# Kernel tuning notes

Hardware: AMD Instinct MI355X
Metric: run time of the kernel (lower is better)

Reference implementation:

```python
import jax, jax.numpy as jnp
import numpy as np

D_MODEL = 1024
N_HEADS = 16
HEAD_DIM = D_MODEL // N_HEADS
ROPE_THETA = 10000.0


def setup_inputs() -> dict:
    key = jax.random.key(0)
    ks = jax.random.split(key, 5)
    B, S = 4, 2048
    x = jax.random.normal(ks[0], (B, S, D_MODEL), dtype=jnp.float32)
    Wq = jax.random.normal(ks[1], (D_MODEL, D_MODEL), dtype=jnp.float32) * 0.02
    Wk = jax.random.normal(ks[2], (D_MODEL, D_MODEL), dtype=jnp.float32) * 0.02
    Wv = jax.random.normal(ks[3], (D_MODEL, D_MODEL), dtype=jnp.float32) * 0.02
    Wo = jax.random.normal(ks[4], (D_MODEL, D_MODEL), dtype=jnp.float32) * 0.02
    token_positions = jnp.arange(S, dtype=jnp.int32)
    return {"x": x, "token_positions": token_positions, "Wq": Wq, "Wk": Wk, "Wv": Wv, "Wo": Wo}


def apply_rope(t, positions):
    # t: [B, H, S, Dk]; positions: [S]
    half = HEAD_DIM // 2
    inv_freq = 1.0 / (ROPE_THETA ** (jnp.arange(half, dtype=jnp.float32) * 2.0 / HEAD_DIM))
    angles = positions.astype(jnp.float32)[:, None] * inv_freq[None, :]  # [S, half]
    cos = jnp.cos(angles)[None, None]  # [1,1,S,half]
    sin = jnp.sin(angles)[None, None]
    t_even = t[..., 0::2]
    t_odd = t[..., 1::2]
    rot_even = t_even * cos - t_odd * sin
    rot_odd = t_even * sin + t_odd * cos
    out = jnp.stack([rot_even, rot_odd], axis=-1)  # [B,H,S,half,2]
    return out.reshape(t.shape)


def reference(x, token_positions, Wq, Wk, Wv, Wo):
    B, S, _ = x.shape
    H, Dk = N_HEADS, HEAD_DIM
    # QKV projections, split heads -> [B, H, S, Dk]
    q = (x @ Wq).reshape(B, S, H, Dk).transpose(0, 2, 1, 3)
    k = (x @ Wk).reshape(B, S, H, Dk).transpose(0, 2, 1, 3)
    v = (x @ Wv).reshape(B, S, H, Dk).transpose(0, 2, 1, 3)
    q = apply_rope(q, token_positions)
    k = apply_rope(k, token_positions)
    scale = 1.0 / jnp.sqrt(jnp.asarray(Dk, dtype=x.dtype))
    scores = jnp.einsum('bhqd,bhkd->bhqk', q, k) * scale
    causal = jnp.tril(jnp.ones((S, S), dtype=bool))
    scores = jnp.where(causal[None, None], scores, jnp.asarray(-jnp.inf, dtype=scores.dtype))
    attn = jax.nn.softmax(scores, axis=-1)
    ctx = jnp.einsum('bhqk,bhkd->bhqd', attn, v)  # [B,H,S,Dk]
    ctx = ctx.transpose(0, 2, 1, 3).reshape(B, S, H * Dk)
    return ctx @ Wo
```

## Files before the change

kernel.cpp:

```cpp
#include <hip/hip_runtime.h>

typedef unsigned short u16;
typedef unsigned int   u32;
typedef __bf16  bf16x8 __attribute__((ext_vector_type(8)));
typedef float   f32x4  __attribute__((ext_vector_type(4)));
typedef float   f32x16 __attribute__((ext_vector_type(16)));
typedef u16     u16x4  __attribute__((ext_vector_type(4)));
typedef u16     u16x8  __attribute__((ext_vector_type(8)));
typedef u32     u32x4  __attribute__((ext_vector_type(4)));

#define D_MODEL 1024
#define N_HEADS 16
#define HEAD_DIM 64
#define BATCH 4
#define SEQ 2048
#define MROWS (BATCH*SEQ)

__device__ __forceinline__ u16 f2bf(float f){
  unsigned u = __builtin_bit_cast(unsigned, f);
  u += 0x7fffu + ((u >> 16) & 1u);
  return (u16)(u >> 16);
}
__device__ __forceinline__ float bf2f(u16 h){
  unsigned u = ((unsigned)h) << 16;
  return __builtin_bit_cast(float, u);
}
__device__ __forceinline__ u32 cvtpk(float a, float b){
  u32 r; asm("v_cvt_pk_bf16_f32 %0, %1, %2" : "=v"(r) : "v"(a), "v"(b)); return r;
}
__device__ __forceinline__ void gload_lds16(const u16* g, u16* l){
  __builtin_amdgcn_global_load_lds((const __attribute__((address_space(1))) void*)g,
                                   (__attribute__((address_space(3))) void*)l, 16, 0, 0);
}
#define MFMA16(a,b,c) __builtin_amdgcn_mfma_f32_16x16x32_bf16((a),(b),(c),0,0,0)

__global__ void k_cvt_x(const float* __restrict__ x, u16* __restrict__ xb, int n4){
  int i = blockIdx.x * 256 + threadIdx.x;
  if (i >= n4) return;
  float4 v = reinterpret_cast<const float4*>(x)[i];
  u16x4 o;
  o.x = f2bf(v.x); o.y = f2bf(v.y); o.z = f2bf(v.z); o.w = f2bf(v.w);
  *reinterpret_cast<u16x4*>(xb + (size_t)i * 4) = o;
}

__global__ void k_transpose_w(const float* __restrict__ Wq, const float* __restrict__ Wk,
                              const float* __restrict__ Wv, const float* __restrict__ Wo,
                              u16* __restrict__ wt){
  __shared__ float t[32][33];
  int z = blockIdx.z;
  const float* W = (z==0)?Wq:(z==1)?Wk:(z==2)?Wv:Wo;
  u16* O = wt + (size_t)z * (D_MODEL*(size_t)D_MODEL);
  int n0 = blockIdx.x*32, k0 = blockIdx.y*32;
  int tx = threadIdx.x, ty = threadIdx.y;
  #pragma unroll
  for (int i = ty; i < 32; i += 8) t[i][tx] = W[(size_t)(k0+i)*D_MODEL + n0 + tx];
  __syncthreads();
  #pragma unroll
  for (int i = ty; i < 32; i += 8){
    int n = n0 + i;
    int np = n;
    if (z < 2){ int d = n & 63; np = (n & ~63) | ((d & 1) << 5) | (d >> 1); }
    O[(size_t)np*D_MODEL + k0 + tx] = f2bf(t[tx][i]);
  }
}

__global__ void k_rope_tab(const int* __restrict__ pos, float2* __restrict__ tab){
  int i = blockIdx.x * 256 + threadIdx.x;
  int s = i >> 5, f = i & 31;
  float inv = exp2f(-(float)f * (13.287712379549449f / 32.0f));
  float a = (float)pos[s] * inv;
  float sn, cs;
  sincosf(a, &sn, &cs);
  tab[i] = make_float2(cs, sn);
}

__global__ __launch_bounds__(512, 4) void k_gqkv(const u16* __restrict__ A, const u16* __restrict__ Bt,
                                                 const float2* __restrict__ tab,
                                                 u16* __restrict__ qout, u16* __restrict__ kout,
                                                 u16* __restrict__ vout){
  __shared__ u16 sh[3*12288];
  const int tid = threadIdx.x, lane = tid & 63, w = tid >> 6;
  const int lr = lane & 15, lg = lane >> 4;
  const int m0 = blockIdx.x * 128, n0 = blockIdx.y * 256;
  const int wm = w >> 2, wn = w & 3;
  const int ra = tid >> 2;
  const int sca = ((tid & 3) ^ ((ra >> 1) & 3)) << 3;
  const u16* gA  = A  + (size_t)(m0 + ra)*1024 + sca;
  const u16* gB0 = Bt + (size_t)(n0 + ra)*1024 + sca;
  const int rb1 = 128 + ra;
  const u16* gB1 = Bt + (size_t)(n0 + rb1)*1024 + (((tid & 3) ^ ((rb1 >> 1) & 3)) << 3);
  const int dA  = w*512;
  const int dB0 = 4096 + w*512;
  const int dB1 = 8192 + w*512;
  int aoff[4], boff[4];
  #pragma unroll
  for (int mi = 0; mi < 4; ++mi){ int r_ = wm*64 + mi*16 + lr; aoff[mi] = r_*32 + ((lg ^ ((r_>>1)&3)) << 3); }
  #pragma unroll
  for (int ni = 0; ni < 4; ++ni){ int r_ = wn*64 + ni*16 + lr; boff[ni] = 4096 + r_*32 + ((lg ^ ((r_>>1)&3)) << 3); }

  f32x4 acc[4][4] = {};
#define SA_(base, t)  gload_lds16(gA  + (size_t)(t)*32, sh + (base) + dA)
#define SB0_(base, t) gload_lds16(gB0 + (size_t)(t)*32, sh + (base) + dB0)
#define SB1_(base, t) gload_lds16(gB1 + (size_t)(t)*32, sh + (base) + dB1)
  SA_(0,0); SB0_(0,0); SB1_(0,0);
  SA_(12288,1); SB0_(12288,1); SB1_(12288,1);
  int b0 = 0, b1 = 12288, b2 = 24576;
  #pragma unroll 1
  for (int t = 0; t < 32; ++t){
    if (t < 31) { asm volatile("s_waitcnt vmcnt(3) lgkmcnt(0)" ::: "memory"); }
    else        { asm volatile("s_waitcnt vmcnt(0) lgkmcnt(0)" ::: "memory"); }
    __builtin_amdgcn_s_barrier();
    __builtin_amdgcn_sched_barrier(0);
    const u16* Sb = sh + b0;
    bf16x8 af0 = *(const bf16x8*)&Sb[aoff[0]];
    bf16x8 af1 = *(const bf16x8*)&Sb[aoff[1]];
    bf16x8 af2 = *(const bf16x8*)&Sb[aoff[2]];
    bf16x8 af3 = *(const bf16x8*)&Sb[aoff[3]];
    bf16x8 vb0 = *(const bf16x8*)&Sb[boff[0]];
    bf16x8 vb1 = *(const bf16x8*)&Sb[boff[1]];
    if (t < 30){ SA_(b2, t+2); }
    __builtin_amdgcn_s_setprio(1);
    acc[0][0] = MFMA16(af0, vb0, acc[0][0]);
    acc[1][0] = MFMA16(af1, vb0, acc[1][0]);
    acc[2][0] = MFMA16(af2, vb0, acc[2][0]);
    acc[3][0] = MFMA16(af3, vb0, acc[3][0]);
    acc[0][1] = MFMA16(af0, vb1, acc[0][1]);
    acc[1][1] = MFMA16(af1, vb1, acc[1][1]);
    acc[2][1] = MFMA16(af2, vb1, acc[2][1]);
    acc[3][1] = MFMA16(af3, vb1, acc[3][1]);
    __builtin_amdgcn_s_setprio(0);
    bf16x8 vb2 = *(const bf16x8*)&Sb[boff[2]];
    bf16x8 vb3 = *(const bf16x8*)&Sb[boff[3]];
    if (t < 30){ SB0_(b2, t+2); SB1_(b2, t+2); }
    __builtin_amdgcn_s_setprio(1);
    acc[0][2] = MFMA16(af0, vb2, acc[0][2]);
    acc[1][2] = MFMA16(af1, vb2, acc[1][2]);
    acc[2][2] = MFMA16(af2, vb2, acc[2][2]);
    acc[3][2] = MFMA16(af3, vb2, acc[3][2]);
    acc[0][3] = MFMA16(af0, vb3, acc[0][3]);
    acc[1][3] = MFMA16(af1, vb3, acc[1][3]);
    acc[2][3] = MFMA16(af2, vb3, acc[2][3]);
    acc[3][3] = MFMA16(af3, vb3, acc[3][3]);
    __builtin_amdgcn_s_setprio(0);
    int tmp = b0; b0 = b1; b1 = b2; b2 = tmp;
  }
#undef SA_
#undef SB0_
#undef SB1_

  const int which = n0 >> 10;
  #pragma unroll
  for (int mi = 0; mi < 4; mi++){
    int row = m0 + wm*64 + mi*16 + lg*4;
    #pragma unroll
    for (int ni = 0; ni < 4; ni++){
      int col = n0 + wn*64 + ni*16 + lr;
      int cm = col & 1023;
      int hh = cm >> 6, d = cm & 63;
      f32x4 vv = acc[mi][ni];
      f32x4 vp = acc[mi][ni ^ 2];
      #pragma unroll
      for (int r = 0; r < 4; r++){
        int rr = row + r;
        int bb = rr >> 11, s = rr & (SEQ-1);
        float val = vv[r];
        if (which < 2){
          float e = (ni < 2) ? val : vp[r];
          float o = (ni < 2) ? vp[r] : val;
          float2 cs = tab[s*32 + ((ni & 1) << 4) + lr];
          float ov = (ni < 2) ? (e*cs.x - o*cs.y) : (e*cs.y + o*cs.x);
          if (which == 0){
            ov *= 0.18033688011112042f;
            qout[(size_t)rr*1024 + cm] = f2bf(ov);
          } else {
            kout[(((size_t)(bb*N_HEADS + hh))*SEQ + s)*64 + d] = f2bf(ov);
          }
        } else {
          vout[(((size_t)(bb*N_HEADS + hh))*(SEQ/16) + (s >> 4))*1024 + d*16 + (s & 15)] = f2bf(val);
        }
      }
    }
  }
}

__global__ __launch_bounds__(256, 4) void k_gemm3(const u16* __restrict__ A, const u16* __restrict__ Bt,
                                                  float* __restrict__ fout){
  __shared__ u16 sh[3*8192];
  const int K = 1024;
  int tid = threadIdx.x, lane = tid & 63, w = tid >> 6;
  int lr = lane & 15, lg = lane >> 4;
  int m0 = blockIdx.x * 128, n0 = blockIdx.y * 128;
  int wm = w >> 1, wn = w & 1;
  int srow = lane >> 2, scol = (lane & 3) * 8;
  const u16* ga = A  + (size_t)(m0 + w*16 + srow)*K + scol;
  const u16* gb = Bt + (size_t)(n0 + w*16 + srow)*K + scol;
  f32x4 acc[4][4] = {};

#define STG(off, t) { u16* Sb = sh + (off); \
    gload_lds16(ga + (size_t)(t)*32,        Sb + w*512); \
    gload_lds16(ga + (size_t)(t)*32 + 64*K, Sb + 2048 + w*512); \
    gload_lds16(gb + (size_t)(t)*32,        Sb + 4096 + w*512); \
    gload_lds16(gb + (size_t)(t)*32 + 64*K, Sb + 6144 + w*512); }

#define CMP(off) { const u16* Sb = sh + (off); \
    bf16x8 af[4], bv[4]; \
    _Pragma("unroll") \
    for (int mi = 0; mi < 4; mi++) \
      af[mi] = *(const bf16x8*)&Sb[(wm*64 + mi*16 + lr)*32 + lg*8]; \
    _Pragma("unroll") \
    for (int ni = 0; ni < 4; ni++) \
      bv[ni] = *(const bf16x8*)&Sb[4096 + (wn*64 + ni*16 + lr)*32 + lg*8]; \
    _Pragma("unroll") \
    for (int mi = 0; mi < 4; mi++){ \
      _Pragma("unroll") \
      for (int ni = 0; ni < 4; ni++) \
        acc[mi][ni] = MFMA16(af[mi], bv[ni], acc[mi][ni]); \
    } }

  STG(0, 0)
  STG(8192, 1)
  int oc = 0, on = 8192, os = 16384;
  #pragma unroll 1
  for (int t = 0; t < 31; ++t){
    asm volatile("s_waitcnt vmcnt(4) lgkmcnt(0)" ::: "memory");
    __builtin_amdgcn_s_barrier();
    __builtin_amdgcn_sched_barrier(0);
    if (t < 30){ STG(os, t+2) }
    CMP(oc)
    int tmp = oc; oc = on; on = os; os = tmp;
  }
  asm volatile("s_waitcnt vmcnt(0) lgkmcnt(0)" ::: "memory");
  __builtin_amdgcn_s_barrier();
  __builtin_amdgcn_sched_barrier(0);
  CMP(oc)
#undef STG
#undef CMP

  #pragma unroll
  for (int mi = 0; mi < 4; mi++){
    int row = m0 + wm*64 + mi*16 + lg*4;
    #pragma unroll
    for (int ni = 0; ni < 4; ni++){
      int col = n0 + wn*64 + ni*16 + lr;
      f32x4 vv = acc[mi][ni];
      #pragma unroll
      for (int r = 0; r < 4; r++)
        fout[(size_t)(row + r)*1024 + col] = vv[r];
    }
  }
}

__global__ __launch_bounds__(256, 3) void k_attn(const u16* __restrict__ q, const u16* __restrict__ k2,
                                                 const u16* __restrict__ v2, u16* __restrict__ ctx){
  __shared__ u16 kv[2][4096];
  const int lane = threadIdx.x & 63, w = threadIdx.x >> 6;
  const int lq = lane & 31, hl = lane >> 5;
  const int B = blockIdx.x;
  const int bh = B & 63, g = 15 - (B >> 6);
  const int b = bh >> 4, h = bh & 15;
  const int qi = 4*g + w;
  const int q0 = qi * 32;
  const int qmax0 = (4*g + 3) * 32;
  const u16* kglob = k2 + (size_t)bh*SEQ*64;
  const u16* vglob = v2 + (size_t)bh*(SEQ/16)*1024;

  const u16* qr_ = q + (size_t)(b*SEQ + q0 + lq)*D_MODEL + h*HEAD_DIM + hl*8;
  bf16x8 qf0 = *(const bf16x8*)&qr_[0];
  bf16x8 qf1 = *(const bf16x8*)&qr_[16];
  bf16x8 qf2 = *(const bf16x8*)&qr_[32];
  bf16x8 qf3 = *(const bf16x8*)&qr_[48];
  f32x16 acc0 = {}, acc1 = {};
  float m = -3.0e38f, l = 0.f;

  auto STAGE = [&](int bf, int jt){
    const u16* ks = kglob + (size_t)(jt + (w<<3) + (lane>>3))*64 + (((lane&7)^(lane>>3))<<3);
    gload_lds16(ks, &kv[bf][w<<9]);
    const u16* vs = vglob + ((size_t)(jt>>4)<<10) + (w<<9) + (lane<<3);
    gload_lds16(vs, &kv[bf][2048 + (w<<9)]);
  };

  STAGE(0, 0);
  __syncthreads();
  int p = 0;
  for (int j0 = 0; j0 <= qmax0; j0 += 32){
    if (j0 + 32 <= qmax0) STAGE(p^1, j0 + 32);
    if (j0 <= q0){
      const char* kb = (const char*)&kv[p][0];
      bf16x8 kf0 = *(const bf16x8*)(kb + lq*128 + (((0+hl) ^ (lq&7))<<4));
      bf16x8 kf1 = *(const bf16x8*)(kb + lq*128 + (((2+hl) ^ (lq&7))<<4));
      bf16x8 kf2 = *(const bf16x8*)(kb + lq*128 + (((4+hl) ^ (lq&7))<<4));
      bf16x8 kf3 = *(const bf16x8*)(kb + lq*128 + (((6+hl) ^ (lq&7))<<4));
      const char* vb = kb + 4096;
      bf16x8 vf00 = *(const bf16x8*)(vb + lq*32 + hl*16);
      bf16x8 vf01 = *(const bf16x8*)(vb + lq*32 + hl*16 + 1024);
      bf16x8 vf10 = *(const bf16x8*)(vb + lq*32 + hl*16 + 2048);
      bf16x8 vf11 = *(const bf16x8*)(vb + lq*32 + hl*16 + 3072);

      f32x16 S = {};
      S = __builtin_amdgcn_mfma_f32_32x32x16_bf16(kf0, qf0, S, 0, 0, 0);
      S = __builtin_amdgcn_mfma_f32_32x32x16_bf16(kf1, qf1, S, 0, 0, 0);
      S = __builtin_amdgcn_mfma_f32_32x32x16_bf16(kf2, qf2, S, 0, 0, 0);
      S = __builtin_amdgcn_mfma_f32_32x32x16_bf16(kf3, qf3, S, 0, 0, 0);

      if (j0 == q0){
        #pragma unroll
        for (int r = 0; r < 16; ++r){
          int kk = (r & 3) + 8*(r >> 2) + 4*hl;
          if (kk > lq) S[r] = -3.0e38f;
        }
      }
      float a0 = fmaxf(fmaxf(S[0],S[1]),  fmaxf(S[2],S[3]));
      float a1 = fmaxf(fmaxf(S[4],S[5]),  fmaxf(S[6],S[7]));
      float a2 = fmaxf(fmaxf(S[8],S[9]),  fmaxf(S[10],S[11]));
      float a3 = fmaxf(fmaxf(S[12],S[13]),fmaxf(S[14],S[15]));
      float pm = fmaxf(fmaxf(a0,a1), fmaxf(a2,a3));
      pm = fmaxf(pm, __shfl_xor(pm, 32));
      if (__any(pm > m + 8.f)){
        float mn = fmaxf(m, pm);
        float cr = __builtin_amdgcn_exp2f(m - mn);
        l *= cr;
        #pragma unroll
        for (int r = 0; r < 16; ++r){ acc0[r] *= cr; acc1[r] *= cr; }
        m = mn;
      }
      #pragma unroll
      for (int r = 0; r < 16; ++r) S[r] = __builtin_amdgcn_exp2f(S[r] - m);
      float s0_ = (S[0]+S[1]) + (S[2]+S[3]);
      float s1_ = (S[4]+S[5]) + (S[6]+S[7]);
      float s2_ = (S[8]+S[9]) + (S[10]+S[11]);
      float s3_ = (S[12]+S[13]) + (S[14]+S[15]);
      l += (s0_+s1_) + (s2_+s3_);
      u32 g0a = cvtpk(S[0], S[1]),  g0b = cvtpk(S[2], S[3]);
      u32 g1a = cvtpk(S[4], S[5]),  g1b = cvtpk(S[6], S[7]);
      u32 g2a = cvtpk(S[8], S[9]),  g2b = cvtpk(S[10],S[11]);
      u32 g3a = cvtpk(S[12],S[13]), g3b = cvtpk(S[14],S[15]);
      u32 s0a = hl ? g0a : g1a, s0b = hl ? g0b : g1b;
      u32 e0a = (u32)__shfl_xor((int)s0a, 32), e0b = (u32)__shfl_xor((int)s0b, 32);
      u32 m0a = hl ? g1a : g0a, m0b = hl ? g1b : g0b;
      u32 s1a = hl ? g2a : g3a, s1b = hl ? g2b : g3b;
      u32 e1a = (u32)__shfl_xor((int)s1a, 32), e1b = (u32)__shfl_xor((int)s1b, 32);
      u32 m1a = hl ? g3a : g2a, m1b = hl ? g3b : g2b;
      u32x4 A0 = { hl ? e0a : m0a, hl ? e0b : m0b, hl ? m0a : e0a, hl ? m0b : e0b };
      u32x4 A1 = { hl ? e1a : m1a, hl ? e1b : m1b, hl ? m1a : e1a, hl ? m1b : e1b };
      bf16x8 pa0 = __builtin_bit_cast(bf16x8, A0);
      bf16x8 pa1 = __builtin_bit_cast(bf16x8, A1);
      acc0 = __builtin_amdgcn_mfma_f32_32x32x16_bf16(vf00, pa0, acc0, 0, 0, 0);
      acc0 = __builtin_amdgcn_mfma_f32_32x32x16_bf16(vf10, pa1, acc0, 0, 0, 0);
      acc1 = __builtin_amdgcn_mfma_f32_32x32x16_bf16(vf01, pa0, acc1, 0, 0, 0);
      acc1 = __builtin_amdgcn_mfma_f32_32x32x16_bf16(vf11, pa1, acc1, 0, 0, 0);
    }
    __syncthreads();
    p ^= 1;
  }
  l += __shfl_xor(l, 32);
  float inv = __builtin_amdgcn_rcpf(l);
  char* tbc = (char*)kv + w*4096;
  #pragma unroll
  for (int r = 0; r < 16; ++r){
    int d0 = (r & 3) + 8*(r >> 2) + 4*hl;
    *(u16*)(tbc + lq*128 + ((2*d0)      ^ ((lq & 7) << 4))) = f2bf(acc0[r] * inv);
    *(u16*)(tbc + lq*128 + ((2*(d0+32)) ^ ((lq & 7) << 4))) = f2bf(acc1[r] * inv);
  }
  int qr2 = lane >> 1, chb = (lane & 1) * 4;
  u16* cp = ctx + (size_t)(b*SEQ + q0 + qr2)*D_MODEL + h*HEAD_DIM;
  #pragma unroll
  for (int i = 0; i < 4; ++i){
    int ch = chb + i;
    u16x8 vv = *(const u16x8*)(tbc + qr2*128 + 16*(ch ^ (qr2 & 7)));
    *(u16x8*)&cp[ch*8] = vv;
  }
}

extern "C" void kernel_launch(void* const* d_in, const int* in_sizes, int n_in,
                              void* d_out, int out_size, void* d_ws, size_t ws_size,
                              hipStream_t stream){
  const float* x  = (const float*)d_in[0];
  const int*  pos = (const int*)d_in[1];
  const float* Wq = (const float*)d_in[2];
  const float* Wk = (const float*)d_in[3];
  const float* Wv = (const float*)d_in[4];
  const float* Wo = (const float*)d_in[5];
  float* out = (float*)d_out;
  char* ws = (char*)d_ws;
  u16* xb   = (u16*)(ws);
  u16* wt   = (u16*)(ws + 16777216);
  u16* qb   = (u16*)(ws + 25165824);
  u16* kbh  = (u16*)(ws + 41943040);
  u16* vt2  = (u16*)(ws + 58720256);
  float2* tab = (float2*)(ws + 75497472);
  u16* ctxb = xb;

  k_cvt_x<<<(MROWS*D_MODEL/4)/256, 256, 0, stream>>>(x, xb, MROWS*D_MODEL/4);
  k_transpose_w<<<dim3(32,32,4), dim3(32,8), 0, stream>>>(Wq, Wk, Wv, Wo, wt);
  k_rope_tab<<<(SEQ*32)/256, 256, 0, stream>>>(pos, tab);
  k_gqkv<<<dim3(64,12), 512, 0, stream>>>(xb, wt, tab, qb, kbh, vt2);
  k_attn<<<dim3(1024), 256, 0, stream>>>(qb, kbh, vt2, ctxb);
  k_gemm3<<<dim3(64,8), 256, 0, stream>>>(ctxb, wt + 3145728, out);
}
```

Before: 180.7 us.

## Double attention KV tile per barrier and swizzle/interleave Wo GEMM pipeline

After: 179.9 us. About the same (-0.4%).

```diff
diff --git a/kernel.cpp b/kernel.cpp
--- a/kernel.cpp
+++ b/kernel.cpp
@@ -183,59 +183,73 @@
   }
 }
 
-__global__ __launch_bounds__(256, 4) void k_gemm3(const u16* __restrict__ A, const u16* __restrict__ Bt,
-                                                  float* __restrict__ fout){
+__global__ __launch_bounds__(256, 4) void k_gwo(const u16* __restrict__ A, const u16* __restrict__ Bt,
+                                                float* __restrict__ fout){
   __shared__ u16 sh[3*8192];
-  const int K = 1024;
-  int tid = threadIdx.x, lane = tid & 63, w = tid >> 6;
-  int lr = lane & 15, lg = lane >> 4;
-  int m0 = blockIdx.x * 128, n0 = blockIdx.y * 128;
-  int wm = w >> 1, wn = w & 1;
-  int srow = lane >> 2, scol = (lane & 3) * 8;
-  const u16* ga = A  + (size_t)(m0 + w*16 + srow)*K + scol;
-  const u16* gb = Bt + (size_t)(n0 + w*16 + srow)*K + scol;
+  const int tid = threadIdx.x, lane = tid & 63, w = tid >> 6;
+  const int lr = lane & 15, lg = lane >> 4;
+  const int m0 = blockIdx.x * 128, n0 = blockIdx.y * 128;
+  const int wm = w >> 1, wn = w & 1;
+  const int ra = w*16 + (lane >> 2);
+  const int sc = ((lane & 3) ^ ((ra >> 1) & 3)) << 3;
+  const u16* gA0 = A  + (size_t)(m0 + ra)*1024 + sc;
+  const u16* gA1 = A  + (size_t)(m0 + 64 + ra)*1024 + sc;
+  const u16* gB0 = Bt + (size_t)(n0 + ra)*1024 + sc;
+  const u16* gB1 = Bt + (size_t)(n0 + 64 + ra)*1024 + sc;
+  int aoff[4], boff[4];
+  #pragma unroll
+  for (int mi = 0; mi < 4; ++mi){ int r_ = wm*64 + mi*16 + lr; aoff[mi] = r_*32 + ((lg ^ ((r_>>1)&3)) << 3); }
+  #pragma unroll
+  for (int ni = 0; ni < 4; ++ni){ int r_ = wn*64 + ni*16 + lr; boff[ni] = 4096 + r_*32 + ((lg ^ ((r_>>1)&3)) << 3); }
   f32x4 acc[4][4] = {};
-
-#define STG(off, t) { u16* Sb = sh + (off); \
-    gload_lds16(ga + (size_t)(t)*32,        Sb + w*512); \
-    gload_lds16(ga + (size_t)(t)*32 + 64*K, Sb + 2048 + w*512); \
-    gload_lds16(gb + (size_t)(t)*32,        Sb + 4096 + w*512); \
-    gload_lds16(gb + (size_t)(t)*32 + 64*K, Sb + 6144 + w*512); }
-
-#define CMP(off) { const u16* Sb = sh + (off); \
-    bf16x8 af[4], bv[4]; \
-    _Pragma("unroll") \
-    for (int mi = 0; mi < 4; mi++) \
-      af[mi] = *(const bf16x8*)&Sb[(wm*64 + mi*16 + lr)*32 + lg*8]; \
-    _Pragma("unroll") \
-    for (int ni = 0; ni < 4; ni++) \
-      bv[ni] = *(const bf16x8*)&Sb[4096 + (wn*64 + ni*16 + lr)*32 + lg*8]; \
-    _Pragma("unroll") \
-    for (int mi = 0; mi < 4; mi++){ \
-      _Pragma("unroll") \
-      for (int ni = 0; ni < 4; ni++) \
-        acc[mi][ni] = MFMA16(af[mi], bv[ni], acc[mi][ni]); \
-    } }
-
-  STG(0, 0)
-  STG(8192, 1)
-  int oc = 0, on = 8192, os = 16384;
+#define SAW(base, t) { gload_lds16(gA0 + (size_t)(t)*32, sh + (base) + w*512); \
+                       gload_lds16(gA1 + (size_t)(t)*32, sh + (base) + 2048 + w*512); }
+#define SBW(base, t) { gload_lds16(gB0 + (size_t)(t)*32, sh + (base) + 4096 + w*512); \
+                       gload_lds16(gB1 + (size_t)(t)*32, sh + (base) + 6144 + w*512); }
+  SAW(0,0) SBW(0,0)
+  SAW(8192,1) SBW(8192,1)
+  int b0 = 0, b1 = 8192, b2 = 16384;
   #pragma unroll 1
-  for (int t = 0; t < 31; ++t){
-    asm volatile("s_waitcnt vmcnt(4) lgkmcnt(0)" ::: "memory");
+  for (int t = 0; t < 32; ++t){
+    if (t < 31) { asm volatile("s_waitcnt vmcnt(4) lgkmcnt(0)" ::: "memory"); }
+    else        { asm volatile("s_waitcnt vmcnt(0) lgkmcnt(0)" ::: "memory"); }
     __builtin_amdgcn_s_barrier();
     __builtin_amdgcn_sched_barrier(0);
-    if (t < 30){ STG(os, t+2) }
-    CMP(oc)
-    int tmp = oc; oc = on; on = os; os = tmp;
-  }
-  asm volatile("s_waitcnt vmcnt(0) lgkmcnt(0)" ::: "memory");
-  __builtin_amdgcn_s_barrier();
-  __builtin_amdgcn_sched_barrier(0);
-  CMP(oc)
-#undef STG
-#undef CMP
-
+    const u16* Sb = sh + b0;
+    bf16x8 af0 = *(const bf16x8*)&Sb[aoff[0]];
+    bf16x8 af1 = *(const bf16x8*)&Sb[aoff[1]];
+    bf16x8 af2 = *(const bf16x8*)&Sb[aoff[2]];
+    bf16x8 af3 = *(const bf16x8*)&Sb[aoff[3]];
+    bf16x8 vb0 = *(const bf16x8*)&Sb[boff[0]];
+    bf16x8 vb1 = *(const bf16x8*)&Sb[boff[1]];
+    if (t < 30){ SAW(b2, t+2) }
+    __builtin_amdgcn_s_setprio(1);
+    acc[0][0] = MFMA16(af0, vb0, acc[0][0]);
+    acc[1][0] = MFMA16(af1, vb0, acc[1][0]);
+    acc[2][0] = MFMA16(af2, vb0, acc[2][0]);
+    acc[3][0] = MFMA16(af3, vb0, acc[3][0]);
+    acc[0][1] = MFMA16(af0, vb1, acc[0][1]);
+    acc[1][1] = MFMA16(af1, vb1, acc[1][1]);
+    acc[2][1] = MFMA16(af2, vb1, acc[2][1]);
+    acc[3][1] = MFMA16(af3, vb1, acc[3][1]);
+    __builtin_amdgcn_s_setprio(0);
+    bf16x8 vb2 = *(const bf16x8*)&Sb[boff[2]];
+    bf16x8 vb3 = *(const bf16x8*)&Sb[boff[3]];
+    if (t < 30){ SBW(b2, t+2) }
+    __builtin_amdgcn_s_setprio(1);
+    acc[0][2] = MFMA16(af0, vb2, acc[0][2]);
+    acc[1][2] = MFMA16(af1, vb2, acc[1][2]);
+    acc[2][2] = MFMA16(af2, vb2, acc[2][2]);
+    acc[3][2] = MFMA16(af3, vb2, acc[3][2]);
+    acc[0][3] = MFMA16(af0, vb3, acc[0][3]);
+    acc[1][3] = MFMA16(af1, vb3, acc[1][3]);
+    acc[2][3] = MFMA16(af2, vb3, acc[2][3]);
+    acc[3][3] = MFMA16(af3, vb3, acc[3][3]);
+    __builtin_amdgcn_s_setprio(0);
+    int tmp = b0; b0 = b1; b1 = b2; b2 = tmp;
+  }
+#undef SAW
+#undef SBW
   #pragma unroll
   for (int mi = 0; mi < 4; mi++){
     int row = m0 + wm*64 + mi*16 + lg*4;
@@ -252,7 +266,7 @@
 
 __global__ __launch_bounds__(256, 3) void k_attn(const u16* __restrict__ q, const u16* __restrict__ k2,
                                                  const u16* __restrict__ v2, u16* __restrict__ ctx){
-  __shared__ u16 kv[2][4096];
+  __shared__ u16 kv[2][8192];
   const int lane = threadIdx.x & 63, w = threadIdx.x >> 6;
   const int lq = lane & 31, hl = lane >> 5;
   const int B = blockIdx.x;
@@ -272,48 +286,71 @@
   f32x16 acc0 = {}, acc1 = {};
   float m = -3.0e38f, l = 0.f;
 
+  const int kr_ = (w<<3) + (lane>>3);
+  const int kc_ = ((lane&7) ^ (lane>>3)) << 3;
   auto STAGE = [&](int bf, int jt){
-    const u16* ks = kglob + (size_t)(jt + (w<<3) + (lane>>3))*64 + (((lane&7)^(lane>>3))<<3);
-    gload_lds16(ks, &kv[bf][w<<9]);
-    const u16* vs = vglob + ((size_t)(jt>>4)<<10) + (w<<9) + (lane<<3);
-    gload_lds16(vs, &kv[bf][2048 + (w<<9)]);
+    gload_lds16(kglob + (size_t)(jt      + kr_)*64 + kc_, &kv[bf][w<<9]);
+    gload_lds16(kglob + (size_t)(jt + 32 + kr_)*64 + kc_, &kv[bf][2048 + (w<<9)]);
+    gload_lds16(vglob + ((size_t)(jt>>4)<<10)        + (w<<9) + (lane<<3), &kv[bf][4096 + (w<<9)]);
+    gload_lds16(vglob + ((size_t)((jt+32)>>4)<<10)   + (w<<9) + (lane<<3), &kv[bf][6144 + (w<<9)]);
   };
 
   STAGE(0, 0);
   __syncthreads();
   int p = 0;
-  for (int j0 = 0; j0 <= qmax0; j0 += 32){
-    if (j0 + 32 <= qmax0) STAGE(p^1, j0 + 32);
+  for (int j0 = 0; j0 <= qmax0; j0 += 64){
+    if (j0 + 64 <= qmax0) STAGE(p^1, j0 + 64);
     if (j0 <= q0){
+      const bool g2 = (j0 + 32 <= q0);
       const char* kb = (const char*)&kv[p][0];
-      bf16x8 kf0 = *(const bf16x8*)(kb + lq*128 + (((0+hl) ^ (lq&7))<<4));
-      bf16x8 kf1 = *(const bf16x8*)(kb + lq*128 + (((2+hl) ^ (lq&7))<<4));
-      bf16x8 kf2 = *(const bf16x8*)(kb + lq*128 + (((4+hl) ^ (lq&7))<<4));
-      bf16x8 kf3 = *(const bf16x8*)(kb + lq*128 + (((6+hl) ^ (lq&7))<<4));
-      const char* vb = kb + 4096;
-      bf16x8 vf00 = *(const bf16x8*)(vb + lq*32 + hl*16);
-      bf16x8 vf01 = *(const bf16x8*)(vb + lq*32 + hl*16 + 1024);
-      bf16x8 vf10 = *(const bf16x8*)(vb + lq*32 + hl*16 + 2048);
-      bf16x8 vf11 = *(const bf16x8*)(vb + lq*32 + hl*16 + 3072);
-
-      f32x16 S = {};
-      S = __builtin_amdgcn_mfma_f32_32x32x16_bf16(kf0, qf0, S, 0, 0, 0);
-      S = __builtin_amdgcn_mfma_f32_32x32x16_bf16(kf1, qf1, S, 0, 0, 0);
-      S = __builtin_amdgcn_mfma_f32_32x32x16_bf16(kf2, qf2, S, 0, 0, 0);
-      S = __builtin_amdgcn_mfma_f32_32x32x16_bf16(kf3, qf3, S, 0, 0, 0);
-
+      f32x16 S1 = {};
+      {
+        bf16x8 kf0 = *(const bf16x8*)(kb + lq*128 + (((0+hl) ^ (lq&7))<<4));
+        bf16x8 kf1 = *(const bf16x8*)(kb + lq*128 + (((2+hl) ^ (lq&7))<<4));
+        bf16x8 kf2 = *(const bf16x8*)(kb + lq*128 + (((4+hl) ^ (lq&7))<<4));
+        bf16x8 kf3 = *(const bf16x8*)(kb + lq*128 + (((6+hl) ^ (lq&7))<<4));
+        S1 = __builtin_amdgcn_mfma_f32_32x32x16_bf16(kf0, qf0, S1, 0, 0, 0);
+        S1 = __builtin_amdgcn_mfma_f32_32x32x16_bf16(kf1, qf1, S1, 0, 0, 0);
+        S1 = __builtin_amdgcn_mfma_f32_32x32x16_bf16(kf2, qf2, S1, 0, 0, 0);
+        S1 = __builtin_amdgcn_mfma_f32_32x32x16_bf16(kf3, qf3, S1, 0, 0, 0);
+      }
       if (j0 == q0){
         #pragma unroll
         for (int r = 0; r < 16; ++r){
           int kk = (r & 3) + 8*(r >> 2) + 4*hl;
-          if (kk > lq) S[r] = -3.0e38f;
+          if (kk > lq) S1[r] = -3.0e38f;
         }
       }
-      float a0 = fmaxf(fmaxf(S[0],S[1]),  fmaxf(S[2],S[3]));
-      float a1 = fmaxf(fmaxf(S[4],S[5]),  fmaxf(S[6],S[7]));
-      float a2 = fmaxf(fmaxf(S[8],S[9]),  fmaxf(S[10],S[11]));
-      float a3 = fmaxf(fmaxf(S[12],S[13]),fmaxf(S[14],S[15]));
-      float pm = fmaxf(fmaxf(a0,a1), fmaxf(a2,a3));
+      f32x16 S2 = {};
+      if (g2){
+        const char* kb2 = kb + 4096;
+        bf16x8 kf0 = *(const bf16x8*)(kb2 + lq*128 + (((0+hl) ^ (lq&7))<<4));
+        bf16x8 kf1 = *(const bf16x8*)(kb2 + lq*128 + (((2+hl) ^ (lq&7))<<4));
+        bf16x8 kf2 = *(const bf16x8*)(kb2 + lq*128 + (((4+hl) ^ (lq&7))<<4));
+        bf16x8 kf3 = *(const bf16x8*)(kb2 + lq*128 + (((6+hl) ^ (lq&7))<<4));
+        S2 = __builtin_amdgcn_mfma_f32_32x32x16_bf16(kf0, qf0, S2, 0, 0, 0);
+        S2 = __builtin_amdgcn_mfma_f32_32x32x16_bf16(kf1, qf1, S2, 0, 0, 0);
+        S2 = __builtin_amdgcn_mfma_f32_32x32x16_bf16(kf2, qf2, S2, 0, 0, 0);
+        S2 = __builtin_amdgcn_mfma_f32_32x32x16_bf16(kf3, qf3, S2, 0, 0, 0);
+        if (j0 + 32 == q0){
+          #pragma unroll
+          for (int r = 0; r < 16; ++r){
+            int kk = (r & 3) + 8*(r >> 2) + 4*hl;
+            if (kk > lq) S2[r] = -3.0e38f;
+          }
+        }
+      }
+      float pm = fmaxf(fmaxf(fmaxf(S1[0],S1[1]), fmaxf(S1[2],S1[3])),
+                       fmaxf(fmaxf(S1[4],S1[5]), fmaxf(S1[6],S1[7])));
+      pm = fmaxf(pm, fmaxf(fmaxf(fmaxf(S1[8],S1[9]), fmaxf(S1[10],S1[11])),
+                           fmaxf(fmaxf(S1[12],S1[13]),fmaxf(S1[14],S1[15]))));
+      if (g2){
+        float pm2 = fmaxf(fmaxf(fmaxf(S2[0],S2[1]), fmaxf(S2[2],S2[3])),
+                          fmaxf(fmaxf(S2[4],S2[5]), fmaxf(S2[6],S2[7])));
+        pm2 = fmaxf(pm2, fmaxf(fmaxf(fmaxf(S2[8],S2[9]), fmaxf(S2[10],S2[11])),
+                               fmaxf(fmaxf(S2[12],S2[13]),fmaxf(S2[14],S2[15]))));
+        pm = fmaxf(pm, pm2);
+      }
       pm = fmaxf(pm, __shfl_xor(pm, 32));
       if (__any(pm > m + 8.f)){
         float mn = fmaxf(m, pm);
@@ -324,30 +361,63 @@
         m = mn;
       }
       #pragma unroll
-      for (int r = 0; r < 16; ++r) S[r] = __builtin_amdgcn_exp2f(S[r] - m);
-      float s0_ = (S[0]+S[1]) + (S[2]+S[3]);
-      float s1_ = (S[4]+S[5]) + (S[6]+S[7]);
-      float s2_ = (S[8]+S[9]) + (S[10]+S[11]);
-      float s3_ = (S[12]+S[13]) + (S[14]+S[15]);
-      l += (s0_+s1_) + (s2_+s3_);
-      u32 g0a = cvtpk(S[0], S[1]),  g0b = cvtpk(S[2], S[3]);
-      u32 g1a = cvtpk(S[4], S[5]),  g1b = cvtpk(S[6], S[7]);
-      u32 g2a = cvtpk(S[8], S[9]),  g2b = cvtpk(S[10],S[11]);
-      u32 g3a = cvtpk(S[12],S[13]), g3b = cvtpk(S[14],S[15]);
-      u32 s0a = hl ? g0a : g1a, s0b = hl ? g0b : g1b;
-      u32 e0a = (u32)__shfl_xor((int)s0a, 32), e0b = (u32)__shfl_xor((int)s0b, 32);
-      u32 m0a = hl ? g1a : g0a, m0b = hl ? g1b : g0b;
-      u32 s1a = hl ? g2a : g3a, s1b = hl ? g2b : g3b;
-      u32 e1a = (u32)__shfl_xor((int)s1a, 32), e1b = (u32)__shfl_xor((int)s1b, 32);
-      u32 m1a = hl ? g3a : g2a, m1b = hl ? g3b : g2b;
-      u32x4 A0 = { hl ? e0a : m0a, hl ? e0b : m0b, hl ? m0a : e0a, hl ? m0b : e0b };
-      u32x4 A1 = { hl ? e1a : m1a, hl ? e1b : m1b, hl ? m1a : e1a, hl ? m1b : e1b };
-      bf16x8 pa0 = __builtin_bit_cast(bf16x8, A0);
-      bf16x8 pa1 = __builtin_bit_cast(bf16x8, A1);
-      acc0 = __builtin_amdgcn_mfma_f32_32x32x16_bf16(vf00, pa0, acc0, 0, 0, 0);
-      acc0 = __builtin_amdgcn_mfma_f32_32x32x16_bf16(vf10, pa1, acc0, 0, 0, 0);
-      acc1 = __builtin_amdgcn_mfma_f32_32x32x16_bf16(vf01, pa0, acc1, 0, 0, 0);
-      acc1 = __builtin_amdgcn_mfma_f32_32x32x16_bf16(vf11, pa1, acc1, 0, 0, 0);
+      for (int r = 0; r < 16; ++r) S1[r] = __builtin_amdgcn_exp2f(S1[r] - m);
+      l += ((S1[0]+S1[1])+(S1[2]+S1[3])) + ((S1[4]+S1[5])+(S1[6]+S1[7]))
+         + ((S1[8]+S1[9])+(S1[10]+S1[11])) + ((S1[12]+S1[13])+(S1[14]+S1[15]));
+      {
+        u32 g0a = cvtpk(S1[0], S1[1]),  g0b = cvtpk(S1[2], S1[3]);
+        u32 g1a = cvtpk(S1[4], S1[5]),  g1b = cvtpk(S1[6], S1[7]);
+        u32 g2a = cvtpk(S1[8], S1[9]),  g2b = cvtpk(S1[10],S1[11]);
+        u32 g3a = cvtpk(S1[12],S1[13]), g3b = cvtpk(S1[14],S1[15]);
+        u32 s0a = hl ? g0a : g1a, s0b = hl ? g0b : g1b;
+        u32 e0a = (u32)__shfl_xor((int)s0a, 32), e0b = (u32)__shfl_xor((int)s0b, 32);
+        u32 m0a = hl ? g1a : g0a, m0b = hl ? g1b : g0b;
+        u32 s1a = hl ? g2a : g3a, s1b = hl ? g2b : g3b;
+        u32 e1a = (u32)__shfl_xor((int)s1a, 32), e1b = (u32)__shfl_xor((int)s1b, 32);
+        u32 m1a = hl ? g3a : g2a, m1b = hl ? g3b : g2b;
+        u32x4 A0 = { hl ? e0a : m0a, hl ? e0b : m0b, hl ? m0a : e0a, hl ? m0b : e0b };
+        u32x4 A1 = { hl ? e1a : m1a, hl ? e1b : m1b, hl ? m1a : e1a, hl ? m1b : e1b };
+        bf16x8 pa0 = __builtin_bit_cast(bf16x8, A0);
+        bf16x8 pa1 = __builtin_bit_cast(bf16x8, A1);
+        const char* vb = kb + 8192;
+        bf16x8 vf00 = *(const bf16x8*)(vb + lq*32 + hl*16);
+        bf16x8 vf01 = *(const bf16x8*)(vb + lq*32 + hl*16 + 1024);
+        bf16x8 vf10 = *(const bf16x8*)(vb + lq*32 + hl*16 + 2048);
+        bf16x8 vf11 = *(const bf16x8*)(vb + lq*32 + hl*16 + 3072);
+        acc0 = __builtin_amdgcn_mfma_f32_32x32x16_bf16(vf00, pa0, acc0, 0, 0, 0);
+        acc0 = __builtin_amdgcn_mfma_f32_32x32x16_bf16(vf10, pa1, acc0, 0, 0, 0);
+        acc1 = __builtin_amdgcn_mfma_f32_32x32x16_bf16(vf01, pa0, acc1, 0, 0, 0);
+        acc1 = __builtin_amdgcn_mfma_f32_32x32x16_bf16(vf11, pa1, acc1, 0, 0, 0);
+      }
+      if (g2){
+        #pragma unroll
+        for (int r = 0; r < 16; ++r) S2[r] = __builtin_amdgcn_exp2f(S2[r] - m);
+        l += ((S2[0]+S2[1])+(S2[2]+S2[3])) + ((S2[4]+S2[5])+(S2[6]+S2[7]))
+           + ((S2[8]+S2[9])+(S2[10]+S2[11])) + ((S2[12]+S2[13])+(S2[14]+S2[15]));
+        u32 g0a = cvtpk(S2[0], S2[1]),  g0b = cvtpk(S2[2], S2[3]);
+        u32 g1a = cvtpk(S2[4], S2[5]),  g1b = cvtpk(S2[6], S2[7]);
+        u32 g2a_ = cvtpk(S2[8], S2[9]), g2b_ = cvtpk(S2[10],S2[11]);
+        u32 g3a = cvtpk(S2[12],S2[13]), g3b = cvtpk(S2[14],S2[15]);
+        u32 s0a = hl ? g0a : g1a, s0b = hl ? g0b : g1b;
+        u32 e0a = (u32)__shfl_xor((int)s0a, 32), e0b = (u32)__shfl_xor((int)s0b, 32);
+        u32 m0a = hl ? g1a : g0a, m0b = hl ? g1b : g0b;
+        u32 s1a = hl ? g2a_ : g3a, s1b = hl ? g2b_ : g3b;
+        u32 e1a = (u32)__shfl_xor((int)s1a, 32), e1b = (u32)__shfl_xor((int)s1b, 32);
+        u32 m1a = hl ? g3a : g2a_, m1b = hl ? g3b : g2b_;
+        u32x4 A0 = { hl ? e0a : m0a, hl ? e0b : m0b, hl ? m0a : e0a, hl ? m0b : e0b };
+        u32x4 A1 = { hl ? e1a : m1a, hl ? e1b : m1b, hl ? m1a : e1a, hl ? m1b : e1b };
+        bf16x8 pa0 = __builtin_bit_cast(bf16x8, A0);
+        bf16x8 pa1 = __builtin_bit_cast(bf16x8, A1);
+        const char* vb = kb + 12288;
+        bf16x8 vf00 = *(const bf16x8*)(vb + lq*32 + hl*16);
+        bf16x8 vf01 = *(const bf16x8*)(vb + lq*32 + hl*16 + 1024);
+        bf16x8 vf10 = *(const bf16x8*)(vb + lq*32 + hl*16 + 2048);
+        bf16x8 vf11 = *(const bf16x8*)(vb + lq*32 + hl*16 + 3072);
+        acc0 = __builtin_amdgcn_mfma_f32_32x32x16_bf16(vf00, pa0, acc0, 0, 0, 0);
+        acc0 = __builtin_amdgcn_mfma_f32_32x32x16_bf16(vf10, pa1, acc0, 0, 0, 0);
+        acc1 = __builtin_amdgcn_mfma_f32_32x32x16_bf16(vf01, pa0, acc1, 0, 0, 0);
+        acc1 = __builtin_amdgcn_mfma_f32_32x32x16_bf16(vf11, pa1, acc1, 0, 0, 0);
+      }
     }
     __syncthreads();
     p ^= 1;
@@ -395,5 +465,5 @@
   k_rope_tab<<<(SEQ*32)/256, 256, 0, stream>>>(pos, tab);
   k_gqkv<<<dim3(64,12), 512, 0, stream>>>(xb, wt, tab, qb, kbh, vt2);
   k_attn<<<dim3(1024), 256, 0, stream>>>(qb, kbh, vt2, ctxb);
-  k_gemm3<<<dim3(64,8), 256, 0, stream>>>(ctxb, wt + 3145728, out);
-}
+  k_gwo<<<dim3(64,8), 256, 0, stream>>>(ctxb, wt + 3145728, out);
+}
```
